# Performance work log

Measured on AMD Instinct MI355X. Metric: run time of the kernel, lower is better.

Reference implementation:

```python
import jax, jax.numpy as jnp
import numpy as np

DIM = 256


def setup_inputs() -> dict:
    key = jax.random.key(0)
    ks = jax.random.split(key, 10)
    d = DIM
    inp = {
        "agent": jax.random.normal(ks[0], (64, d), dtype=jnp.float32),
        "x": jax.random.normal(ks[1], (8, 4096, d), dtype=jnp.float32),
        # parameters (stored as [in, out]; y = x @ W + b)
        "W_qkv": jax.random.normal(ks[2], (d, 3 * d), dtype=jnp.float32) * (d ** -0.5),
        "b_qkv": jnp.zeros((3 * d,), dtype=jnp.float32),
        "W_agent": jax.random.normal(ks[3], (d, 2 * d), dtype=jnp.float32) * (d ** -0.5),
        "b_agent": jnp.zeros((2 * d,), dtype=jnp.float32),
        "W_fc1": jax.random.normal(ks[4], (d, d), dtype=jnp.float32) * (d ** -0.5),
        "b_fc1": jnp.zeros((d,), dtype=jnp.float32),
        "W_fc2": jax.random.normal(ks[5], (d, d), dtype=jnp.float32) * (d ** -0.5),
        "b_fc2": jnp.zeros((d,), dtype=jnp.float32),
    }
    return inp


def reference(agent, x, W_qkv, b_qkv, W_agent, b_agent, W_fc1, b_fc1, W_fc2, b_fc2):
    d = x.shape[-1]
    scale = d ** -0.5
    # qkv projection of tokens: [B,N,3d] -> q,k,v each [B,N,d]
    qkv = x @ W_qkv + b_qkv
    q, k, v = jnp.split(qkv, 3, axis=-1)
    # agent projection: [K,2d] -> q_agent,k_agent each [K,d]
    ag = agent @ W_agent + b_agent
    q_agent, k_agent = jnp.split(ag, 2, axis=-1)
    # stage 1: agents attend over tokens -> [B,K,N]
    attn1 = jax.nn.softmax(jnp.einsum('kd,bnd->bkn', q_agent, k) * scale, axis=-1)
    va = jnp.einsum('bkn,bnd->bkd', attn1, v)  # [B,K,d]
    va = va @ W_fc1 + b_fc1
    # stage 2: tokens attend over agents -> [B,N,K]
    attn2 = jax.nn.softmax(jnp.einsum('bnd,kd->bnk', q, k_agent) * scale, axis=-1)
    out = jnp.einsum('bnk,bkd->bnd', attn2, va)  # [B,N,d]
    out = out @ W_fc2 + b_fc2
    return out + x
```

## Files before the change

### kernel.cpp

```cpp
#include <hip/hip_runtime.h>
#include <stdint.h>
#include <string.h>

#define BB 8
#define NN 4096
#define DD 256
#define SCALE 0.0625f
#define XS 264

using frag_ab = __attribute__((ext_vector_type(8))) short;
using frag_cd = __attribute__((ext_vector_type(4))) float;

__device__ __forceinline__ unsigned short f2bf(float f) {
    union { float f; unsigned u; } a; a.f = f;
    unsigned r = a.u + 0x7FFFu + ((a.u >> 16) & 1u);
    return (unsigned short)(r >> 16);
}

__global__ __launch_bounds__(256) void k_setup1(
    const float* __restrict__ agent, const float* __restrict__ Wag,
    const float* __restrict__ bag, float* __restrict__ ag,
    const float* __restrict__ Wqkv, const float* __restrict__ Wfc1,
    const float* __restrict__ bqkv, const float* __restrict__ bfc1,
    float* __restrict__ T, float* __restrict__ Tb)
{
    __shared__ float sh[256];
    const int bx = blockIdx.x, tid = threadIdx.x;
    if (bx < 64) {
        sh[tid] = agent[bx * 256 + tid];
        __syncthreads();
#pragma unroll
        for (int h = 0; h < 2; ++h) {
            int j = tid + h * 256;
            float s = bag[j];
            for (int kk = 0; kk < 256; ++kk) s += sh[kk] * Wag[kk * 512 + j];
            ag[bx * 512 + j] = s;
        }
    } else {
        const int i = bx - 64;
        sh[tid] = Wqkv[i * 768 + 512 + tid];
        __syncthreads();
        float s = 0.f;
        for (int o = 0; o < 256; ++o) s += sh[o] * Wfc1[o * 256 + tid];
        T[i * 256 + tid] = s;
        if (i == 0) {
            float t = bfc1[tid];
            for (int o = 0; o < 256; ++o) t += bqkv[512 + o] * Wfc1[o * 256 + tid];
            Tb[tid] = t;
        }
    }
}

__global__ __launch_bounds__(256) void k_setup2(
    const float* __restrict__ ag, const float* __restrict__ Wqkv,
    const float* __restrict__ bqkv, unsigned short* __restrict__ P12t,
    float* __restrict__ c12, const float* __restrict__ T,
    const float* __restrict__ Tb, const float* __restrict__ Wfc2,
    float* __restrict__ W3, float* __restrict__ b3)
{
    __shared__ float arow[256];
    __shared__ float red[256];
    const int bx = blockIdx.x, tid = threadIdx.x;
    if (bx < 128) {
        const int c = bx;
        const int woff = (c < 64) ? 256 : 0;
        const int aoff = (c < 64) ? 0 : 256;
        const int row = c & 63;
        arow[tid] = ag[row * 512 + aoff + tid];
        __syncthreads();
        float s = 0.f;
        for (int o = 0; o < 256; ++o) s += Wqkv[tid * 768 + woff + o] * arow[o];
        P12t[(size_t)c * 256 + tid] = f2bf(SCALE * s);
        red[tid] = bqkv[woff + tid] * arow[tid];
        __syncthreads();
        for (int st = 128; st; st >>= 1) {
            if (tid < st) red[tid] += red[tid + st];
            __syncthreads();
        }
        if (tid == 0) c12[c] = SCALE * red[0];
    } else {
        const int i = bx - 128;
        arow[tid] = T[i * 256 + tid];
        __syncthreads();
        float s = 0.f;
        for (int k = 0; k < 256; ++k) s += arow[k] * Wfc2[k * 256 + tid];
        W3[i * 256 + tid] = s;
        if (i == 0) {
            float t = 0.f;
            for (int k = 0; k < 256; ++k) t += Tb[k] * Wfc2[k * 256 + tid];
            b3[tid] = t;
        }
    }
}

__global__ __launch_bounds__(256) void k_xlogits(
    const float* __restrict__ x, const unsigned short* __restrict__ P12t,
    const float* __restrict__ c12, unsigned short* __restrict__ xt,
    float* __restrict__ l1, unsigned short* __restrict__ p2b,
    float* __restrict__ statM, float* __restrict__ statS)
{
    __shared__ unsigned short xtile[64 * XS];
    __shared__ unsigned short Bs[128 * 72];
    __shared__ float Sm[4][64], Ss[4][64], Cm[64];
    const int chunk = blockIdx.x, b = blockIdx.y;
    const int n0 = chunk * 64;
    const int tid = threadIdx.x;
    const int w = tid >> 6, lane = tid & 63;
    const int ml = lane & 15, q = lane >> 4;

#pragma unroll
    for (int p = 0; p < 16; ++p) {
        int idx = p * 256 + tid;
        int tok = idx >> 6, d = (idx & 63) * 4;
        float4 v = *(const float4*)&x[(size_t)(b * 4096 + n0 + tok) * 256 + d];
        unsigned short u[4] = {f2bf(v.x), f2bf(v.y), f2bf(v.z), f2bf(v.w)};
        uint2 pk; memcpy(&pk, u, 8);
        *(uint2*)&xtile[tok * XS + d] = pk;
    }
    __syncthreads();
#pragma unroll
    for (int p = 0; p < 16; ++p) {
        int idx = p * 256 + tid;
        int d = idx >> 4, seg = idx & 15;
        unsigned short u[4];
#pragma unroll
        for (int k = 0; k < 4; ++k) u[k] = xtile[(seg * 4 + k) * XS + d];
        uint2 pk; memcpy(&pk, u, 8);
        *(uint2*)&xt[(size_t)(b * 256 + d) * 4096 + n0 + seg * 4] = pk;
    }

    frag_cd acc[8];
#pragma unroll
    for (int j = 0; j < 8; ++j)
#pragma unroll
        for (int r = 0; r < 4; ++r) acc[j][r] = 0.f;

    for (int kb = 0; kb < 256; kb += 64) {
        __syncthreads();
#pragma unroll
        for (int p = 0; p < 4; ++p) {
            int idx = p * 256 + tid;
            int r = idx >> 3, c = (idx & 7) * 8;
            *(uint4*)&Bs[r * 72 + c] = *(const uint4*)&P12t[(size_t)r * 256 + kb + c];
        }
        __syncthreads();
#pragma unroll
        for (int ks = 0; ks < 2; ++ks) {
            const int kk = ks * 32 + q * 8;
            frag_ab a = *(const frag_ab*)&xtile[(w * 16 + ml) * XS + kb + kk];
#pragma unroll
            for (int j = 0; j < 8; ++j) {
                frag_ab bf = *(const frag_ab*)&Bs[(j * 16 + ml) * 72 + kk];
                acc[j] = __builtin_amdgcn_mfma_f32_16x16x32_bf16(a, bf, acc[j], 0, 0, 0);
            }
        }
    }

#pragma unroll
    for (int j = 0; j < 4; ++j) {
        *(float4*)&l1[(size_t)(b * 64 + j * 16 + ml) * 4096 + n0 + w * 16 + q * 4] =
            make_float4(acc[j][0], acc[j][1], acc[j][2], acc[j][3]);
        float m = fmaxf(fmaxf(acc[j][0], acc[j][1]), fmaxf(acc[j][2], acc[j][3]));
        m = fmaxf(m, __shfl_xor(m, 16));
        m = fmaxf(m, __shfl_xor(m, 32));
        if (q == 0) Sm[w][j * 16 + ml] = m;
    }
    __syncthreads();
    if (tid < 64)
        Cm[tid] = fmaxf(fmaxf(Sm[0][tid], Sm[1][tid]), fmaxf(Sm[2][tid], Sm[3][tid]));
    __syncthreads();
#pragma unroll
    for (int j = 0; j < 4; ++j) {
        float cm = Cm[j * 16 + ml];
        float s = __expf(acc[j][0] - cm) + __expf(acc[j][1] - cm) +
                  __expf(acc[j][2] - cm) + __expf(acc[j][3] - cm);
        s += __shfl_xor(s, 16);
        s += __shfl_xor(s, 32);
        if (q == 0) Ss[w][j * 16 + ml] = s;
    }
    __syncthreads();
    if (tid < 64) {
        size_t si = (size_t)(b * 64 + tid) * 64 + chunk;
        statM[si] = Cm[tid];
        statS[si] = Ss[0][tid] + Ss[1][tid] + Ss[2][tid] + Ss[3][tid];
    }

    float v[4][4], cc[4];
#pragma unroll
    for (int jj = 0; jj < 4; ++jj) {
        cc[jj] = c12[64 + jj * 16 + ml];
#pragma unroll
        for (int r = 0; r < 4; ++r) v[jj][r] = acc[4 + jj][r] + cc[jj];
    }
#pragma unroll
    for (int r = 0; r < 4; ++r) {
        float m = fmaxf(fmaxf(v[0][r], v[1][r]), fmaxf(v[2][r], v[3][r]));
#pragma unroll
        for (int mask = 1; mask <= 8; mask <<= 1) m = fmaxf(m, __shfl_xor(m, mask));
        float e[4], s = 0.f;
#pragma unroll
        for (int jj = 0; jj < 4; ++jj) { e[jj] = __expf(v[jj][r] - m); s += e[jj]; }
#pragma unroll
        for (int mask = 1; mask <= 8; mask <<= 1) s += __shfl_xor(s, mask);
        float inv = 1.f / s;
        size_t base = (size_t)(b * 4096 + n0 + w * 16 + q * 4 + r) * 64;
#pragma unroll
        for (int jj = 0; jj < 4; ++jj)
            p2b[base + jj * 16 + ml] = f2bf(e[jj] * inv);
    }
}

__global__ __launch_bounds__(256) void k_va(
    const float* __restrict__ l1, const float* __restrict__ statM,
    const float* __restrict__ statS, const unsigned short* __restrict__ xt,
    unsigned short* __restrict__ part)
{
    __shared__ unsigned short As[64 * 144];
    __shared__ unsigned short Bs[128 * 144];
    __shared__ float Rm[4][64], Rs[4][64], rowM[64], rowInv[64];
    const int s = blockIdx.x, dh = blockIdx.y, b = blockIdx.z;
    const int tid = threadIdx.x;
    const int w = tid >> 6, lane = tid & 63;
    const int ml = lane & 15, q = lane >> 4;

#pragma unroll
    for (int p = 0; p < 8; ++p) {
        int idx = p * 256 + tid;
        int r = idx >> 4, c = (idx & 15) * 8;
        *(uint4*)&Bs[r * 144 + c] =
            *(const uint4*)&xt[(size_t)(b * 256 + dh * 128 + r) * 4096 + s * 128 + c];
    }

    const int a = tid & 63, qq = tid >> 6;
    float pm[16], ps[16];
    {
        const float* pmp = &statM[(size_t)(b * 64 + a) * 64 + qq * 16];
        const float* psp = &statS[(size_t)(b * 64 + a) * 64 + qq * 16];
#pragma unroll
        for (int p = 0; p < 4; ++p) {
            float4 m4 = *(const float4*)&pmp[p * 4];
            float4 s4 = *(const float4*)&psp[p * 4];
            pm[p * 4 + 0] = m4.x; pm[p * 4 + 1] = m4.y; pm[p * 4 + 2] = m4.z; pm[p * 4 + 3] = m4.w;
            ps[p * 4 + 0] = s4.x; ps[p * 4 + 1] = s4.y; ps[p * 4 + 2] = s4.z; ps[p * 4 + 3] = s4.w;
        }
        float m = -INFINITY;
#pragma unroll
        for (int i = 0; i < 16; ++i) m = fmaxf(m, pm[i]);
        Rm[qq][a] = m;
    }
    __syncthreads();
    {
        float M = fmaxf(fmaxf(Rm[0][a], Rm[1][a]), fmaxf(Rm[2][a], Rm[3][a]));
        float sum = 0.f;
#pragma unroll
        for (int i = 0; i < 16; ++i) sum += ps[i] * __expf(pm[i] - M);
        Rs[qq][a] = sum;
        if (qq == 0) rowM[a] = M;
    }
    __syncthreads();
    if (tid < 64)
        rowInv[tid] = 1.f / (Rs[0][tid] + Rs[1][tid] + Rs[2][tid] + Rs[3][tid]);
    __syncthreads();

#pragma unroll
    for (int p = 0; p < 8; ++p) {
        int idx = (p * 256 + tid) * 4;
        int ag = idx >> 7, t = idx & 127;
        float4 lv = *(const float4*)&l1[(size_t)(b * 64 + ag) * 4096 + s * 128 + t];
        float M = rowM[ag], inv = rowInv[ag];
        unsigned short u[4] = {f2bf(__expf(lv.x - M) * inv), f2bf(__expf(lv.y - M) * inv),
                               f2bf(__expf(lv.z - M) * inv), f2bf(__expf(lv.w - M) * inv)};
        uint2 pk; memcpy(&pk, u, 8);
        *(uint2*)&As[ag * 144 + t] = pk;
    }
    __syncthreads();

    frag_cd acc[4][2];
#pragma unroll
    for (int i = 0; i < 4; ++i)
#pragma unroll
        for (int j = 0; j < 2; ++j)
#pragma unroll
            for (int r = 0; r < 4; ++r) acc[i][j][r] = 0.f;
#pragma unroll
    for (int ks = 0; ks < 4; ++ks) {
        const int kk = ks * 32 + q * 8;
        frag_ab af[4];
#pragma unroll
        for (int i = 0; i < 4; ++i)
            af[i] = *(const frag_ab*)&As[(i * 16 + ml) * 144 + kk];
#pragma unroll
        for (int j = 0; j < 2; ++j) {
            frag_ab bf = *(const frag_ab*)&Bs[(w * 32 + j * 16 + ml) * 144 + kk];
#pragma unroll
            for (int i = 0; i < 4; ++i)
                acc[i][j] = __builtin_amdgcn_mfma_f32_16x16x32_bf16(
                    af[i], bf, acc[i][j], 0, 0, 0);
        }
    }
#pragma unroll
    for (int i = 0; i < 4; ++i)
#pragma unroll
        for (int j = 0; j < 2; ++j) {
            int d = dh * 128 + w * 32 + j * 16 + ml;
#pragma unroll
            for (int r = 0; r < 4; ++r)
                part[(size_t)((s * 8 + b) * 64 + i * 16 + q * 4 + r) * 256 + d] =
                    f2bf(acc[i][j][r]);
        }
}

__global__ __launch_bounds__(256) void k_fc(
    const unsigned short* __restrict__ part, const float* __restrict__ W3,
    const float* __restrict__ b3, unsigned short* __restrict__ va3t)
{
    __shared__ float rowb[256];
    const int row = blockIdx.x, tid = threadIdx.x;
    const int b = row >> 6, agc = row & 63;
    float sv = 0.f;
    for (int s = 0; s < 32; ++s) {
        union { unsigned u; float f; } cv;
        cv.u = ((unsigned)part[(size_t)((s * 8 + b) * 64 + agc) * 256 + tid]) << 16;
        sv += cv.f;
    }
    rowb[tid] = sv;
    __syncthreads();
    float s2 = b3[tid];
    for (int k = 0; k < 256; ++k) s2 += rowb[k] * W3[k * 256 + tid];
    va3t[(size_t)(b * 256 + tid) * 64 + agc] = f2bf(s2);
}

__global__ __launch_bounds__(256) void k_stage2(
    const unsigned short* __restrict__ p2b, const unsigned short* __restrict__ va3t,
    const float* __restrict__ x, const float* __restrict__ bfc2,
    float* __restrict__ out)
{
    __shared__ unsigned short Ps[64 * 72];
    __shared__ unsigned short Vs[256 * 72];
    const int n0 = blockIdx.x * 64, b = blockIdx.y;
    const int tid = threadIdx.x;
    const int w = tid >> 6, lane = tid & 63;
    const int ml = lane & 15, q = lane >> 4;

#pragma unroll
    for (int p = 0; p < 8; ++p) {
        int idx = p * 256 + tid;
        int r = idx >> 3, c = (idx & 7) * 8;
        *(uint4*)&Vs[r * 72 + c] =
            *(const uint4*)&va3t[(size_t)(b * 256 + r) * 64 + c];
    }
#pragma unroll
    for (int p = 0; p < 2; ++p) {
        int idx = p * 256 + tid;
        int r = idx >> 3, c = (idx & 7) * 8;
        *(uint4*)&Ps[r * 72 + c] =
            *(const uint4*)&p2b[(size_t)(b * 4096 + n0 + r) * 64 + c];
    }
    __syncthreads();

    frag_cd acc[4][4];
#pragma unroll
    for (int i = 0; i < 4; ++i)
#pragma unroll
        for (int j = 0; j < 4; ++j)
#pragma unroll
            for (int r = 0; r < 4; ++r) acc[i][j][r] = 0.f;
#pragma unroll
    for (int ks = 0; ks < 2; ++ks) {
        const int kk = ks * 32 + q * 8;
        frag_ab bf[4];
#pragma unroll
        for (int j = 0; j < 4; ++j)
            bf[j] = *(const frag_ab*)&Vs[(w * 64 + j * 16 + ml) * 72 + kk];
#pragma unroll
        for (int i = 0; i < 4; ++i) {
            frag_ab a = *(const frag_ab*)&Ps[(i * 16 + ml) * 72 + kk];
#pragma unroll
            for (int j = 0; j < 4; ++j)
                acc[i][j] = __builtin_amdgcn_mfma_f32_16x16x32_bf16(
                    a, bf[j], acc[i][j], 0, 0, 0);
        }
    }

    float bias[4];
#pragma unroll
    for (int j = 0; j < 4; ++j) bias[j] = bfc2[w * 64 + j * 16 + ml];
#pragma unroll
    for (int i = 0; i < 4; ++i) {
        size_t base = ((size_t)b * 4096 + n0 + i * 16 + q * 4) * 256;
#pragma unroll
        for (int j = 0; j < 4; ++j) {
            int d = w * 64 + j * 16 + ml;
#pragma unroll
            for (int r = 0; r < 4; ++r) {
                size_t ad = base + (size_t)r * 256 + d;
                out[ad] = acc[i][j][r] + bias[j] + x[ad];
            }
        }
    }
}

extern "C" void kernel_launch(void* const* d_in, const int* in_sizes, int n_in,
                              void* d_out, int out_size, void* d_ws, size_t ws_size,
                              hipStream_t stream) {
    const float* agent = (const float*)d_in[0];
    const float* x     = (const float*)d_in[1];
    const float* Wqkv  = (const float*)d_in[2];
    const float* bqkv  = (const float*)d_in[3];
    const float* Wag   = (const float*)d_in[4];
    const float* bag   = (const float*)d_in[5];
    const float* Wfc1  = (const float*)d_in[6];
    const float* bfc1  = (const float*)d_in[7];
    const float* Wfc2  = (const float*)d_in[8];
    const float* bfc2  = (const float*)d_in[9];
    float* out = (float*)d_out;

    char* w = (char*)d_ws;
    size_t off = 0;
    unsigned short* xt   = (unsigned short*)(w + off); off += (size_t)BB * DD * NN * 2;
    float* l1   = (float*)(w + off); off += (size_t)BB * 64 * NN * 4;
    unsigned short* p2b  = (unsigned short*)(w + off); off += (size_t)BB * NN * 64 * 2;
    unsigned short* part = (unsigned short*)(w + off); off += (size_t)32 * BB * 64 * 256 * 2;
    float* ag   = (float*)(w + off); off += (size_t)64 * 512 * 4;
    float* T    = (float*)(w + off); off += (size_t)256 * 256 * 4;
    float* Tb   = (float*)(w + off); off += 256 * 4;
    unsigned short* P12t = (unsigned short*)(w + off); off += (size_t)128 * 256 * 2;
    float* c12  = (float*)(w + off); off += 128 * 4;
    float* W3   = (float*)(w + off); off += (size_t)256 * 256 * 4;
    float* b3   = (float*)(w + off); off += 256 * 4;
    float* statM = (float*)(w + off); off += (size_t)BB * 64 * 64 * 4;
    float* statS = (float*)(w + off); off += (size_t)BB * 64 * 64 * 4;
    unsigned short* va3t = (unsigned short*)(w + off); off += (size_t)BB * DD * 64 * 2;

    k_setup1<<<320, 256, 0, stream>>>(agent, Wag, bag, ag, Wqkv, Wfc1, bqkv, bfc1, T, Tb);
    k_setup2<<<384, 256, 0, stream>>>(ag, Wqkv, bqkv, P12t, c12, T, Tb, Wfc2, W3, b3);
    k_xlogits<<<dim3(64, BB), 256, 0, stream>>>(x, P12t, c12, xt, l1, p2b, statM, statS);
    k_va<<<dim3(32, 2, BB), 256, 0, stream>>>(l1, statM, statS, xt, part);
    k_fc<<<512, 256, 0, stream>>>(part, W3, b3, va3t);
    k_stage2<<<dim3(64, BB), 256, 0, stream>>>(p2b, va3t, x, bfc2, out);
}
```

Before: 169.3 us.

## Merge setup kernels, drop softmax max pass, store bf16 exp logits

The two setup kernels become one, and the weight products W3 are stored in bf16. The stage-1 softmax now skips max-subtraction, so k_xlogits writes bf16 exp values and per-chunk sums instead of fp32 logits plus max/sum statistics. Work is also retiled: smaller token chunks and more blocks in k_xlogits and k_va, and vectorized float4 residual stores in stage2. Dropping the max pass cuts a statistics pass and halves logit traffic, but exponentials can overflow if logits are large.

```diff
diff --git a/kernel.cpp b/kernel.cpp
--- a/kernel.cpp
+++ b/kernel.cpp
@@ -6,7 +6,7 @@
 #define NN 4096
 #define DD 256
 #define SCALE 0.0625f
-#define XS 264
+#define XS2 264
 
 using frag_ab = __attribute__((ext_vector_type(8))) short;
 using frag_cd = __attribute__((ext_vector_type(4))) float;
@@ -16,47 +16,18 @@
     unsigned r = a.u + 0x7FFFu + ((a.u >> 16) & 1u);
     return (unsigned short)(r >> 16);
 }
-
-__global__ __launch_bounds__(256) void k_setup1(
+__device__ __forceinline__ float bf2f(unsigned short h) {
+    union { unsigned u; float f; } a; a.u = ((unsigned)h) << 16;
+    return a.f;
+}
+
+__global__ __launch_bounds__(256) void k_setup(
     const float* __restrict__ agent, const float* __restrict__ Wag,
-    const float* __restrict__ bag, float* __restrict__ ag,
-    const float* __restrict__ Wqkv, const float* __restrict__ Wfc1,
-    const float* __restrict__ bqkv, const float* __restrict__ bfc1,
-    float* __restrict__ T, float* __restrict__ Tb)
-{
-    __shared__ float sh[256];
-    const int bx = blockIdx.x, tid = threadIdx.x;
-    if (bx < 64) {
-        sh[tid] = agent[bx * 256 + tid];
-        __syncthreads();
-#pragma unroll
-        for (int h = 0; h < 2; ++h) {
-            int j = tid + h * 256;
-            float s = bag[j];
-            for (int kk = 0; kk < 256; ++kk) s += sh[kk] * Wag[kk * 512 + j];
-            ag[bx * 512 + j] = s;
-        }
-    } else {
-        const int i = bx - 64;
-        sh[tid] = Wqkv[i * 768 + 512 + tid];
-        __syncthreads();
-        float s = 0.f;
-        for (int o = 0; o < 256; ++o) s += sh[o] * Wfc1[o * 256 + tid];
-        T[i * 256 + tid] = s;
-        if (i == 0) {
-            float t = bfc1[tid];
-            for (int o = 0; o < 256; ++o) t += bqkv[512 + o] * Wfc1[o * 256 + tid];
-            Tb[tid] = t;
-        }
-    }
-}
-
-__global__ __launch_bounds__(256) void k_setup2(
-    const float* __restrict__ ag, const float* __restrict__ Wqkv,
-    const float* __restrict__ bqkv, unsigned short* __restrict__ P12t,
-    float* __restrict__ c12, const float* __restrict__ T,
-    const float* __restrict__ Tb, const float* __restrict__ Wfc2,
-    float* __restrict__ W3, float* __restrict__ b3)
+    const float* __restrict__ bag, const float* __restrict__ Wqkv,
+    const float* __restrict__ bqkv, const float* __restrict__ Wfc1,
+    const float* __restrict__ bfc1, const float* __restrict__ Wfc2,
+    unsigned short* __restrict__ P12t, float* __restrict__ c2,
+    unsigned short* __restrict__ W3b, float* __restrict__ b3)
 {
     __shared__ float arow[256];
     __shared__ float red[256];
@@ -66,72 +37,82 @@
         const int woff = (c < 64) ? 256 : 0;
         const int aoff = (c < 64) ? 0 : 256;
         const int row = c & 63;
-        arow[tid] = ag[row * 512 + aoff + tid];
-        __syncthreads();
-        float s = 0.f;
-        for (int o = 0; o < 256; ++o) s += Wqkv[tid * 768 + woff + o] * arow[o];
-        P12t[(size_t)c * 256 + tid] = f2bf(SCALE * s);
-        red[tid] = bqkv[woff + tid] * arow[tid];
-        __syncthreads();
-        for (int st = 128; st; st >>= 1) {
-            if (tid < st) red[tid] += red[tid + st];
+        float s = bag[aoff + tid];
+        for (int o = 0; o < 256; ++o) s += agent[row * 256 + o] * Wag[o * 512 + aoff + tid];
+        arow[tid] = s;
+        __syncthreads();
+        float p = 0.f;
+        for (int o = 0; o < 256; ++o) p += Wqkv[tid * 768 + woff + o] * arow[o];
+        P12t[(size_t)c * 256 + tid] = f2bf(SCALE * p);
+        if (c >= 64) {
+            red[tid] = bqkv[woff + tid] * arow[tid];
             __syncthreads();
-        }
-        if (tid == 0) c12[c] = SCALE * red[0];
+            for (int st = 128; st; st >>= 1) {
+                if (tid < st) red[tid] += red[tid + st];
+                __syncthreads();
+            }
+            if (tid == 0) c2[c - 64] = SCALE * red[0];
+        }
+    } else if (bx < 384) {
+        const int i = bx - 128;
+        float t = 0.f;
+        for (int o = 0; o < 256; ++o) t += Wqkv[i * 768 + 512 + o] * Wfc1[o * 256 + tid];
+        arow[tid] = t;
+        __syncthreads();
+        float p = 0.f;
+        for (int k = 0; k < 256; ++k) p += arow[k] * Wfc2[k * 256 + tid];
+        W3b[(size_t)i * 256 + tid] = f2bf(p);
     } else {
-        const int i = bx - 128;
-        arow[tid] = T[i * 256 + tid];
-        __syncthreads();
-        float s = 0.f;
-        for (int k = 0; k < 256; ++k) s += arow[k] * Wfc2[k * 256 + tid];
-        W3[i * 256 + tid] = s;
-        if (i == 0) {
-            float t = 0.f;
-            for (int k = 0; k < 256; ++k) t += Tb[k] * Wfc2[k * 256 + tid];
-            b3[tid] = t;
-        }
+        float t = bfc1[tid];
+        for (int o = 0; o < 256; ++o) t += bqkv[512 + o] * Wfc1[o * 256 + tid];
+        arow[tid] = t;
+        __syncthreads();
+        float p = 0.f;
+        for (int k = 0; k < 256; ++k) p += arow[k] * Wfc2[k * 256 + tid];
+        b3[tid] = p;
     }
 }
 
 __global__ __launch_bounds__(256) void k_xlogits(
     const float* __restrict__ x, const unsigned short* __restrict__ P12t,
-    const float* __restrict__ c12, unsigned short* __restrict__ xt,
-    float* __restrict__ l1, unsigned short* __restrict__ p2b,
-    float* __restrict__ statM, float* __restrict__ statS)
-{
-    __shared__ unsigned short xtile[64 * XS];
+    const float* __restrict__ c2, unsigned short* __restrict__ xt,
+    unsigned short* __restrict__ p1, unsigned short* __restrict__ p2b,
+    float* __restrict__ statS)
+{
+    __shared__ unsigned short xtile[32 * XS2];
     __shared__ unsigned short Bs[128 * 72];
-    __shared__ float Sm[4][64], Ss[4][64], Cm[64];
+    __shared__ float Ss[2][64];
     const int chunk = blockIdx.x, b = blockIdx.y;
-    const int n0 = chunk * 64;
+    const int n0 = chunk * 32;
     const int tid = threadIdx.x;
     const int w = tid >> 6, lane = tid & 63;
     const int ml = lane & 15, q = lane >> 4;
-
-#pragma unroll
-    for (int p = 0; p < 16; ++p) {
+    const int rt = w & 1, cg = w >> 1;
+
+#pragma unroll
+    for (int p = 0; p < 8; ++p) {
         int idx = p * 256 + tid;
         int tok = idx >> 6, d = (idx & 63) * 4;
         float4 v = *(const float4*)&x[(size_t)(b * 4096 + n0 + tok) * 256 + d];
         unsigned short u[4] = {f2bf(v.x), f2bf(v.y), f2bf(v.z), f2bf(v.w)};
         uint2 pk; memcpy(&pk, u, 8);
-        *(uint2*)&xtile[tok * XS + d] = pk;
-    }
-    __syncthreads();
-#pragma unroll
-    for (int p = 0; p < 16; ++p) {
-        int idx = p * 256 + tid;
-        int d = idx >> 4, seg = idx & 15;
+        *(uint2*)&xtile[tok * XS2 + d] = pk;
+    }
+    __syncthreads();
+#pragma unroll
+    for (int p = 0; p < 8; ++p) {
+        int idx = p * 256 + tid;
+        int d = idx >> 3, seg = idx & 7;
         unsigned short u[4];
 #pragma unroll
-        for (int k = 0; k < 4; ++k) u[k] = xtile[(seg * 4 + k) * XS + d];
+        for (int k = 0; k < 4; ++k) u[k] = xtile[(seg * 4 + k) * XS2 + d];
         uint2 pk; memcpy(&pk, u, 8);
         *(uint2*)&xt[(size_t)(b * 256 + d) * 4096 + n0 + seg * 4] = pk;
     }
 
-    frag_cd acc[8];
-#pragma unroll
-    for (int j = 0; j < 8; ++j)
+    frag_cd acc[4];
+#pragma unroll
+    for (int j = 0; j < 4; ++j)
 #pragma unroll
         for (int r = 0; r < 4; ++r) acc[j][r] = 0.f;
 
@@ -147,186 +128,142 @@
 #pragma unroll
         for (int ks = 0; ks < 2; ++ks) {
             const int kk = ks * 32 + q * 8;
-            frag_ab a = *(const frag_ab*)&xtile[(w * 16 + ml) * XS + kb + kk];
-#pragma unroll
-            for (int j = 0; j < 8; ++j) {
-                frag_ab bf = *(const frag_ab*)&Bs[(j * 16 + ml) * 72 + kk];
+            frag_ab a = *(const frag_ab*)&xtile[(rt * 16 + ml) * XS2 + kb + kk];
+#pragma unroll
+            for (int j = 0; j < 4; ++j) {
+                frag_ab bf = *(const frag_ab*)&Bs[(cg * 64 + j * 16 + ml) * 72 + kk];
                 acc[j] = __builtin_amdgcn_mfma_f32_16x16x32_bf16(a, bf, acc[j], 0, 0, 0);
             }
         }
     }
 
-#pragma unroll
-    for (int j = 0; j < 4; ++j) {
-        *(float4*)&l1[(size_t)(b * 64 + j * 16 + ml) * 4096 + n0 + w * 16 + q * 4] =
-            make_float4(acc[j][0], acc[j][1], acc[j][2], acc[j][3]);
-        float m = fmaxf(fmaxf(acc[j][0], acc[j][1]), fmaxf(acc[j][2], acc[j][3]));
-        m = fmaxf(m, __shfl_xor(m, 16));
-        m = fmaxf(m, __shfl_xor(m, 32));
-        if (q == 0) Sm[w][j * 16 + ml] = m;
+    if (cg == 0) {
+#pragma unroll
+        for (int j = 0; j < 4; ++j) {
+            const int ag = j * 16 + ml;
+            float e[4];
+#pragma unroll
+            for (int r = 0; r < 4; ++r) e[r] = __expf(acc[j][r]);
+            unsigned short u[4] = {f2bf(e[0]), f2bf(e[1]), f2bf(e[2]), f2bf(e[3])};
+            uint2 pk; memcpy(&pk, u, 8);
+            *(uint2*)&p1[(size_t)(b * 64 + ag) * 4096 + n0 + rt * 16 + q * 4] = pk;
+            float s = e[0] + e[1] + e[2] + e[3];
+            s += __shfl_xor(s, 16);
+            s += __shfl_xor(s, 32);
+            if (q == 0) Ss[rt][ag] = s;
+        }
+    } else {
+        float cc[4];
+#pragma unroll
+        for (int j = 0; j < 4; ++j) cc[j] = c2[j * 16 + ml];
+#pragma unroll
+        for (int r = 0; r < 4; ++r) {
+            float e[4], s = 0.f;
+#pragma unroll
+            for (int j = 0; j < 4; ++j) {
+                e[j] = __expf(acc[j][r] + cc[j]);
+                s += e[j];
+            }
+#pragma unroll
+            for (int mask = 1; mask <= 8; mask <<= 1) s += __shfl_xor(s, mask);
+            float inv = 1.f / s;
+            const int tok = n0 + rt * 16 + q * 4 + r;
+#pragma unroll
+            for (int j = 0; j < 4; ++j)
+                p2b[(size_t)(b * 4096 + tok) * 64 + j * 16 + ml] = f2bf(e[j] * inv);
+        }
     }
     __syncthreads();
     if (tid < 64)
-        Cm[tid] = fmaxf(fmaxf(Sm[0][tid], Sm[1][tid]), fmaxf(Sm[2][tid], Sm[3][tid]));
-    __syncthreads();
-#pragma unroll
-    for (int j = 0; j < 4; ++j) {
-        float cm = Cm[j * 16 + ml];
-        float s = __expf(acc[j][0] - cm) + __expf(acc[j][1] - cm) +
-                  __expf(acc[j][2] - cm) + __expf(acc[j][3] - cm);
-        s += __shfl_xor(s, 16);
-        s += __shfl_xor(s, 32);
-        if (q == 0) Ss[w][j * 16 + ml] = s;
-    }
-    __syncthreads();
-    if (tid < 64) {
-        size_t si = (size_t)(b * 64 + tid) * 64 + chunk;
-        statM[si] = Cm[tid];
-        statS[si] = Ss[0][tid] + Ss[1][tid] + Ss[2][tid] + Ss[3][tid];
-    }
-
-    float v[4][4], cc[4];
-#pragma unroll
-    for (int jj = 0; jj < 4; ++jj) {
-        cc[jj] = c12[64 + jj * 16 + ml];
-#pragma unroll
-        for (int r = 0; r < 4; ++r) v[jj][r] = acc[4 + jj][r] + cc[jj];
-    }
-#pragma unroll
-    for (int r = 0; r < 4; ++r) {
-        float m = fmaxf(fmaxf(v[0][r], v[1][r]), fmaxf(v[2][r], v[3][r]));
-#pragma unroll
-        for (int mask = 1; mask <= 8; mask <<= 1) m = fmaxf(m, __shfl_xor(m, mask));
-        float e[4], s = 0.f;
-#pragma unroll
-        for (int jj = 0; jj < 4; ++jj) { e[jj] = __expf(v[jj][r] - m); s += e[jj]; }
-#pragma unroll
-        for (int mask = 1; mask <= 8; mask <<= 1) s += __shfl_xor(s, mask);
-        float inv = 1.f / s;
-        size_t base = (size_t)(b * 4096 + n0 + w * 16 + q * 4 + r) * 64;
-#pragma unroll
-        for (int jj = 0; jj < 4; ++jj)
-            p2b[base + jj * 16 + ml] = f2bf(e[jj] * inv);
-    }
+        statS[(size_t)(b * 64 + tid) * 128 + chunk] = Ss[0][tid] + Ss[1][tid];
 }
 
 __global__ __launch_bounds__(256) void k_va(
-    const float* __restrict__ l1, const float* __restrict__ statM,
-    const float* __restrict__ statS, const unsigned short* __restrict__ xt,
-    unsigned short* __restrict__ part)
-{
-    __shared__ unsigned short As[64 * 144];
-    __shared__ unsigned short Bs[128 * 144];
-    __shared__ float Rm[4][64], Rs[4][64], rowM[64], rowInv[64];
+    const unsigned short* __restrict__ p1, const float* __restrict__ statS,
+    const unsigned short* __restrict__ xt, unsigned short* __restrict__ part)
+{
+    __shared__ unsigned short As[64 * 152];
+    __shared__ unsigned short Bs[64 * 152];
+    __shared__ float Rs[4][64], Inv[64];
     const int s = blockIdx.x, dh = blockIdx.y, b = blockIdx.z;
     const int tid = threadIdx.x;
     const int w = tid >> 6, lane = tid & 63;
     const int ml = lane & 15, q = lane >> 4;
 
 #pragma unroll
+    for (int p = 0; p < 4; ++p) {
+        int idx = p * 256 + tid;
+        int r = idx >> 4, c = (idx & 15) * 8;
+        *(uint4*)&Bs[r * 152 + c] =
+            *(const uint4*)&xt[(size_t)(b * 256 + dh * 64 + r) * 4096 + s * 128 + c];
+    }
+    {
+        const int a = tid & 63, qq = tid >> 6;
+        const float* ps = &statS[(size_t)(b * 64 + a) * 128 + qq * 32];
+        float sum = 0.f;
+#pragma unroll
+        for (int p = 0; p < 8; ++p) {
+            float4 s4 = *(const float4*)&ps[p * 4];
+            sum += s4.x + s4.y + s4.z + s4.w;
+        }
+        Rs[qq][a] = sum;
+    }
+    __syncthreads();
+    if (tid < 64)
+        Inv[tid] = 1.f / (Rs[0][tid] + Rs[1][tid] + Rs[2][tid] + Rs[3][tid]);
+    __syncthreads();
+#pragma unroll
     for (int p = 0; p < 8; ++p) {
-        int idx = p * 256 + tid;
-        int r = idx >> 4, c = (idx & 15) * 8;
-        *(uint4*)&Bs[r * 144 + c] =
-            *(const uint4*)&xt[(size_t)(b * 256 + dh * 128 + r) * 4096 + s * 128 + c];
-    }
-
-    const int a = tid & 63, qq = tid >> 6;
-    float pm[16], ps[16];
-    {
-        const float* pmp = &statM[(size_t)(b * 64 + a) * 64 + qq * 16];
-        const float* psp = &statS[(size_t)(b * 64 + a) * 64 + qq * 16];
-#pragma unroll
-        for (int p = 0; p < 4; ++p) {
-            float4 m4 = *(const float4*)&pmp[p * 4];
-            float4 s4 = *(const float4*)&psp[p * 4];
-            pm[p * 4 + 0] = m4.x; pm[p * 4 + 1] = m4.y; pm[p * 4 + 2] = m4.z; pm[p * 4 + 3] = m4.w;
-            ps[p * 4 + 0] = s4.x; ps[p * 4 + 1] = s4.y; ps[p * 4 + 2] = s4.z; ps[p * 4 + 3] = s4.w;
-        }
-        float m = -INFINITY;
-#pragma unroll
-        for (int i = 0; i < 16; ++i) m = fmaxf(m, pm[i]);
-        Rm[qq][a] = m;
-    }
-    __syncthreads();
-    {
-        float M = fmaxf(fmaxf(Rm[0][a], Rm[1][a]), fmaxf(Rm[2][a], Rm[3][a]));
-        float sum = 0.f;
-#pragma unroll
-        for (int i = 0; i < 16; ++i) sum += ps[i] * __expf(pm[i] - M);
-        Rs[qq][a] = sum;
-        if (qq == 0) rowM[a] = M;
-    }
-    __syncthreads();
-    if (tid < 64)
-        rowInv[tid] = 1.f / (Rs[0][tid] + Rs[1][tid] + Rs[2][tid] + Rs[3][tid]);
-    __syncthreads();
-
-#pragma unroll
-    for (int p = 0; p < 8; ++p) {
-        int idx = (p * 256 + tid) * 4;
-        int ag = idx >> 7, t = idx & 127;
-        float4 lv = *(const float4*)&l1[(size_t)(b * 64 + ag) * 4096 + s * 128 + t];
-        float M = rowM[ag], inv = rowInv[ag];
-        unsigned short u[4] = {f2bf(__expf(lv.x - M) * inv), f2bf(__expf(lv.y - M) * inv),
-                               f2bf(__expf(lv.z - M) * inv), f2bf(__expf(lv.w - M) * inv)};
-        uint2 pk; memcpy(&pk, u, 8);
-        *(uint2*)&As[ag * 144 + t] = pk;
-    }
-    __syncthreads();
-
-    frag_cd acc[4][2];
+        int idx4 = (p * 256 + tid) * 4;
+        int ag = idx4 >> 7, t = idx4 & 127;
+        uint2 pk = *(const uint2*)&p1[(size_t)(b * 64 + ag) * 4096 + s * 128 + t];
+        unsigned short in[4]; memcpy(in, &pk, 8);
+        float inv = Inv[ag];
+        unsigned short u[4] = {f2bf(bf2f(in[0]) * inv), f2bf(bf2f(in[1]) * inv),
+                               f2bf(bf2f(in[2]) * inv), f2bf(bf2f(in[3]) * inv)};
+        uint2 po; memcpy(&po, u, 8);
+        *(uint2*)&As[ag * 152 + t] = po;
+    }
+    __syncthreads();
+
+    frag_cd acc[4];
 #pragma unroll
     for (int i = 0; i < 4; ++i)
 #pragma unroll
-        for (int j = 0; j < 2; ++j)
-#pragma unroll
-            for (int r = 0; r < 4; ++r) acc[i][j][r] = 0.f;
+        for (int r = 0; r < 4; ++r) acc[i][r] = 0.f;
 #pragma unroll
     for (int ks = 0; ks < 4; ++ks) {
         const int kk = ks * 32 + q * 8;
-        frag_ab af[4];
-#pragma unroll
-        for (int i = 0; i < 4; ++i)
-            af[i] = *(const frag_ab*)&As[(i * 16 + ml) * 144 + kk];
-#pragma unroll
-        for (int j = 0; j < 2; ++j) {
-            frag_ab bf = *(const frag_ab*)&Bs[(w * 32 + j * 16 + ml) * 144 + kk];
-#pragma unroll
-            for (int i = 0; i < 4; ++i)
-                acc[i][j] = __builtin_amdgcn_mfma_f32_16x16x32_bf16(
-                    af[i], bf, acc[i][j], 0, 0, 0);
-        }
-    }
+        frag_ab bf = *(const frag_ab*)&Bs[(w * 16 + ml) * 152 + kk];
+#pragma unroll
+        for (int i = 0; i < 4; ++i) {
+            frag_ab a = *(const frag_ab*)&As[(i * 16 + ml) * 152 + kk];
+            acc[i] = __builtin_amdgcn_mfma_f32_16x16x32_bf16(a, bf, acc[i], 0, 0, 0);
+        }
+    }
+    const int d = dh * 64 + w * 16 + ml;
 #pragma unroll
     for (int i = 0; i < 4; ++i)
 #pragma unroll
-        for (int j = 0; j < 2; ++j) {
-            int d = dh * 128 + w * 32 + j * 16 + ml;
-#pragma unroll
-            for (int r = 0; r < 4; ++r)
-                part[(size_t)((s * 8 + b) * 64 + i * 16 + q * 4 + r) * 256 + d] =
-                    f2bf(acc[i][j][r]);
-        }
+        for (int r = 0; r < 4; ++r)
+            part[(size_t)((s * 8 + b) * 64 + i * 16 + q * 4 + r) * 256 + d] =
+                f2bf(acc[i][r]);
 }
 
 __global__ __launch_bounds__(256) void k_fc(
-    const unsigned short* __restrict__ part, const float* __restrict__ W3,
+    const unsigned short* __restrict__ part, const unsigned short* __restrict__ W3b,
     const float* __restrict__ b3, unsigned short* __restrict__ va3t)
 {
     __shared__ float rowb[256];
     const int row = blockIdx.x, tid = threadIdx.x;
     const int b = row >> 6, agc = row & 63;
     float sv = 0.f;
-    for (int s = 0; s < 32; ++s) {
-        union { unsigned u; float f; } cv;
-        cv.u = ((unsigned)part[(size_t)((s * 8 + b) * 64 + agc) * 256 + tid]) << 16;
-        sv += cv.f;
-    }
+    for (int s = 0; s < 32; ++s)
+        sv += bf2f(part[(size_t)((s * 8 + b) * 64 + agc) * 256 + tid]);
     rowb[tid] = sv;
     __syncthreads();
     float s2 = b3[tid];
-    for (int k = 0; k < 256; ++k) s2 += rowb[k] * W3[k * 256 + tid];
+    for (int k = 0; k < 256; ++k) s2 += rowb[k] * bf2f(W3b[(size_t)k * 256 + tid]);
     va3t[(size_t)(b * 256 + tid) * 64 + agc] = f2bf(s2);
 }
 
@@ -335,8 +272,8 @@
     const float* __restrict__ x, const float* __restrict__ bfc2,
     float* __restrict__ out)
 {
+    __shared__ unsigned short Vs[256 * 72];
     __shared__ unsigned short Ps[64 * 72];
-    __shared__ unsigned short Vs[256 * 72];
     const int n0 = blockIdx.x * 64, b = blockIdx.y;
     const int tid = threadIdx.x;
     const int w = tid >> 6, lane = tid & 63;
@@ -346,15 +283,13 @@
     for (int p = 0; p < 8; ++p) {
         int idx = p * 256 + tid;
         int r = idx >> 3, c = (idx & 7) * 8;
-        *(uint4*)&Vs[r * 72 + c] =
-            *(const uint4*)&va3t[(size_t)(b * 256 + r) * 64 + c];
+        *(uint4*)&Vs[r * 72 + c] = *(const uint4*)&va3t[(size_t)(b * 256 + r) * 64 + c];
     }
 #pragma unroll
     for (int p = 0; p < 2; ++p) {
         int idx = p * 256 + tid;
         int r = idx >> 3, c = (idx & 7) * 8;
-        *(uint4*)&Ps[r * 72 + c] =
-            *(const uint4*)&p2b[(size_t)(b * 4096 + n0 + r) * 64 + c];
+        *(uint4*)&Ps[r * 72 + c] = *(const uint4*)&p2b[(size_t)(b * 4096 + n0 + r) * 64 + c];
     }
     __syncthreads();
 
@@ -368,34 +303,36 @@
 #pragma unroll
     for (int ks = 0; ks < 2; ++ks) {
         const int kk = ks * 32 + q * 8;
-        frag_ab bf[4];
+        frag_ab a[4], bf[4];
+#pragma unroll
+        for (int i = 0; i < 4; ++i)
+            a[i] = *(const frag_ab*)&Vs[(w * 64 + i * 16 + ml) * 72 + kk];
 #pragma unroll
         for (int j = 0; j < 4; ++j)
-            bf[j] = *(const frag_ab*)&Vs[(w * 64 + j * 16 + ml) * 72 + kk];
-#pragma unroll
-        for (int i = 0; i < 4; ++i) {
-            frag_ab a = *(const frag_ab*)&Ps[(i * 16 + ml) * 72 + kk];
+            bf[j] = *(const frag_ab*)&Ps[(j * 16 + ml) * 72 + kk];
+#pragma unroll
+        for (int i = 0; i < 4; ++i)
 #pragma unroll
             for (int j = 0; j < 4; ++j)
                 acc[i][j] = __builtin_amdgcn_mfma_f32_16x16x32_bf16(
-                    a, bf[j], acc[i][j], 0, 0, 0);
-        }
-    }
-
-    float bias[4];
-#pragma unroll
-    for (int j = 0; j < 4; ++j) bias[j] = bfc2[w * 64 + j * 16 + ml];
+                    a[i], bf[j], acc[i][j], 0, 0, 0);
+    }
+
 #pragma unroll
     for (int i = 0; i < 4; ++i) {
-        size_t base = ((size_t)b * 4096 + n0 + i * 16 + q * 4) * 256;
+        const int d0 = w * 64 + i * 16 + q * 4;
+        float4 bias = *(const float4*)&bfc2[d0];
 #pragma unroll
         for (int j = 0; j < 4; ++j) {
-            int d = w * 64 + j * 16 + ml;
-#pragma unroll
-            for (int r = 0; r < 4; ++r) {
-                size_t ad = base + (size_t)r * 256 + d;
-                out[ad] = acc[i][j][r] + bias[j] + x[ad];
-            }
+            const int tok = n0 + j * 16 + ml;
+            size_t ad = (size_t)(b * 4096 + tok) * 256 + d0;
+            float4 xr = *(const float4*)&x[ad];
+            float4 o;
+            o.x = acc[i][j][0] + bias.x + xr.x;
+            o.y = acc[i][j][1] + bias.y + xr.y;
+            o.z = acc[i][j][2] + bias.z + xr.z;
+            o.w = acc[i][j][3] + bias.w + xr.w;
+            *(float4*)&out[ad] = o;
         }
     }
 }
@@ -418,24 +355,20 @@
     char* w = (char*)d_ws;
     size_t off = 0;
     unsigned short* xt   = (unsigned short*)(w + off); off += (size_t)BB * DD * NN * 2;
-    float* l1   = (float*)(w + off); off += (size_t)BB * 64 * NN * 4;
+    unsigned short* p1   = (unsigned short*)(w + off); off += (size_t)BB * 64 * NN * 2;
     unsigned short* p2b  = (unsigned short*)(w + off); off += (size_t)BB * NN * 64 * 2;
     unsigned short* part = (unsigned short*)(w + off); off += (size_t)32 * BB * 64 * 256 * 2;
-    float* ag   = (float*)(w + off); off += (size_t)64 * 512 * 4;
-    float* T    = (float*)(w + off); off += (size_t)256 * 256 * 4;
-    float* Tb   = (float*)(w + off); off += 256 * 4;
+    float* statS = (float*)(w + off); off += (size_t)BB * 64 * 128 * 4;
     unsigned short* P12t = (unsigned short*)(w + off); off += (size_t)128 * 256 * 2;
-    float* c12  = (float*)(w + off); off += 128 * 4;
-    float* W3   = (float*)(w + off); off += (size_t)256 * 256 * 4;
+    float* c2   = (float*)(w + off); off += 256 * 4;
+    unsigned short* W3b = (unsigned short*)(w + off); off += (size_t)256 * 256 * 2;
     float* b3   = (float*)(w + off); off += 256 * 4;
-    float* statM = (float*)(w + off); off += (size_t)BB * 64 * 64 * 4;
-    float* statS = (float*)(w + off); off += (size_t)BB * 64 * 64 * 4;
     unsigned short* va3t = (unsigned short*)(w + off); off += (size_t)BB * DD * 64 * 2;
 
-    k_setup1<<<320, 256, 0, stream>>>(agent, Wag, bag, ag, Wqkv, Wfc1, bqkv, bfc1, T, Tb);
-    k_setup2<<<384, 256, 0, stream>>>(ag, Wqkv, bqkv, P12t, c12, T, Tb, Wfc2, W3, b3);
-    k_xlogits<<<dim3(64, BB), 256, 0, stream>>>(x, P12t, c12, xt, l1, p2b, statM, statS);
-    k_va<<<dim3(32, 2, BB), 256, 0, stream>>>(l1, statM, statS, xt, part);
-    k_fc<<<512, 256, 0, stream>>>(part, W3, b3, va3t);
+    k_setup<<<385, 256, 0, stream>>>(agent, Wag, bag, Wqkv, bqkv, Wfc1, bfc1, Wfc2,
+                                     P12t, c2, W3b, b3);
+    k_xlogits<<<dim3(128, BB), 256, 0, stream>>>(x, P12t, c2, xt, p1, p2b, statS);
+    k_va<<<dim3(32, 4, BB), 256, 0, stream>>>(p1, statS, xt, part);
+    k_fc<<<512, 256, 0, stream>>>(part, W3b, b3, va3t);
     k_stage2<<<dim3(64, BB), 256, 0, stream>>>(p2b, va3t, x, bfc2, out);
 }
```

Measured after the change: 169.0 us. No clear change (-0.2%).
